# Performance work log

Measured on AMD Instinct MI355X. Metric: run time of the kernel, lower is better.

The kernel has to match this reference:

```python
import math
import jax, jax.numpy as jnp
import numpy as np

B, L, T, D, H, SD = 8, 512, 512, 768, 12, 5


def setup_inputs() -> dict:
    key = jax.random.key(0)
    ks = jax.random.split(key, 16)
    s = 0.02
    return {
        "q": jax.random.normal(ks[0], (B, L, D), jnp.float32),
        "k": jax.random.normal(ks[1], (B, T, D), jnp.float32),
        "v": jax.random.normal(ks[2], (B, T, D), jnp.float32),
        "pairwise_locs": jax.random.normal(ks[3], (B, L, T, SD), jnp.float32),
        "key_padding_mask": jax.random.randint(ks[4], (B, T), 0, 2).astype(bool),
        "Wq": jax.random.normal(ks[5], (D, D), jnp.float32) * s,
        "bq": jnp.zeros((D,), jnp.float32),
        "Wk": jax.random.normal(ks[6], (D, D), jnp.float32) * s,
        "bk": jnp.zeros((D,), jnp.float32),
        "Wv": jax.random.normal(ks[7], (D, D), jnp.float32) * s,
        "bv": jnp.zeros((D,), jnp.float32),
        "Wl": jax.random.normal(ks[8], (D, H * (SD + 1)), jnp.float32) * s,
        "bl": jnp.zeros((H * (SD + 1),), jnp.float32),
        "Wf": jax.random.normal(ks[9], (D, D), jnp.float32) * s,
        "bf": jnp.zeros((D,), jnp.float32),
    }


def reference(q, k, v, pairwise_locs, key_padding_mask,
              Wq, bq, Wk, bk, Wv, bv, Wl, bl, Wf, bf):
    b, l, d = q.shape
    t = k.shape[1]
    sd = pairwise_locs.shape[-1]
    h = Wl.shape[1] // (sd + 1)          # spatial_multihead=True -> h == n_head
    dh = d // h

    # projections -> [h, b, seq, dh]
    qh = (q @ Wq + bq).reshape(b, l, h, dh).transpose(2, 0, 1, 3)
    kh = (k @ Wk + bk).reshape(b, t, h, dh).transpose(2, 0, 1, 3)
    vh = (v @ Wv + bv).reshape(b, t, h, dh).transpose(2, 0, 1, 3)

    attn = jnp.einsum('hblk,hbtk->hblt', qh, kh) / math.sqrt(dh)

    # language-conditioned spatial weights from residual (= q input)
    sw = (q @ Wl + bl).reshape(b, l, h, sd + 1).transpose(2, 0, 1, 3)  # [h,b,l,sd+1]
    spatial_bias = sw[..., :1]
    spatial_w = sw[..., 1:]
    loc_attn = jax.nn.sigmoid(
        jnp.einsum('hbld,bltd->hblt', spatial_w, pairwise_locs) + spatial_bias)

    mask = key_padding_mask[None, :, None, :]          # [1,b,1,t]
    attn = jnp.where(mask, -jnp.inf, attn)
    loc_attn = jnp.where(mask, 0.0, loc_attn)

    fused_attn = jax.nn.softmax(jnp.log(jnp.clip(loc_attn, 1e-6)) + attn, axis=3)

    out = jnp.einsum('hblt,hbtv->hblv', fused_attn, vh)
    out = out.transpose(1, 2, 0, 3).reshape(b, l, d)
    out = out @ Wf + bf
    return (out, fused_attn)
```

## Files before the change

### kernel.cpp

```cpp
#include <hip/hip_runtime.h>
#include <hip/hip_bf16.h>

#define B_ 8
#define L_ 512
#define T_ 512
#define D_ 768
#define H_ 12
#define DH_ 64
#define SD_ 5
#define NSW_ 72
#define K2_ 1536
#define K3_ 2304

typedef __attribute__((ext_vector_type(8))) short bf16x8;
typedef __attribute__((ext_vector_type(4))) float f32x4;

__device__ __forceinline__ unsigned short f2bf(float x) {
    union { __hip_bfloat16 h; unsigned short u; } cv;
    cv.h = __float2bfloat16(x);
    return cv.u;
}
__device__ __forceinline__ float bf2f(unsigned short u) {
    union { unsigned short u; __hip_bfloat16 h; } cv;
    cv.u = u;
    return __bfloat162float(cv.h);
}

__device__ __forceinline__ void gload_lds16(const void* g, void* l) {
    __builtin_amdgcn_global_load_lds((const __attribute__((address_space(1))) void*)g,
                                     (__attribute__((address_space(3))) void*)l,
                                     16, 0, 0);
}

__global__ __launch_bounds__(256) void asplit_kernel(
    const float* __restrict__ q, const float* __restrict__ k, const float* __restrict__ v,
    short* __restrict__ q2, short* __restrict__ k2, short* __restrict__ v2)
{
    const int z = blockIdx.z;
    const float* A = (z == 0) ? q : (z == 1) ? k : v;
    short* O = (z == 0) ? q2 : (z == 1) ? k2 : v2;
    const int col = blockIdx.x * 256 + threadIdx.x;
    const int m   = blockIdx.y;
    if (col >= D_) return;
    const float a = A[(size_t)m * D_ + col];
    const unsigned short hi = f2bf(a);
    const unsigned short lo = f2bf(a - bf2f(hi));
    O[(size_t)m * K2_ + col]       = (short)hi;
    O[(size_t)m * K2_ + D_ + col]  = (short)lo;
}

__global__ __launch_bounds__(256) void wsplit_kernel(
    const float* __restrict__ Wq, const float* __restrict__ Wk,
    const float* __restrict__ Wv, const float* __restrict__ Wl,
    const float* __restrict__ Wf,
    short* __restrict__ WqT3, short* __restrict__ WkT3, short* __restrict__ WvT3,
    short* __restrict__ WlT3, short* __restrict__ WfT3)
{
    const int z = blockIdx.z;
    const float* W; short* O; int Nw, Npad;
    if (z == 0)      { W = Wq; O = WqT3; Nw = D_;   Npad = 768; }
    else if (z == 1) { W = Wk; O = WkT3; Nw = D_;   Npad = 768; }
    else if (z == 2) { W = Wv; O = WvT3; Nw = D_;   Npad = 768; }
    else if (z == 3) { W = Wl; O = WlT3; Nw = NSW_; Npad = 128; }
    else             { W = Wf; O = WfT3; Nw = D_;   Npad = 768; }

    const int k0 = blockIdx.x * 64;
    const int n0 = blockIdx.y * 64;
    if (n0 >= Npad) return;

    __shared__ float sm[64][65];
    const int c  = threadIdx.x & 63;
    const int r4 = threadIdx.x >> 6;

#pragma unroll
    for (int i = 0; i < 16; i++) {
        const int r = i * 4 + r4;
        float val = 0.f;
        if (n0 + c < Nw) val = W[(size_t)(k0 + r) * Nw + n0 + c];
        sm[r][c] = val;
    }
    __syncthreads();

#pragma unroll
    for (int i = 0; i < 16; i++) {
        const int nl = i * 4 + r4;
        const int n  = n0 + nl;
        if (n >= Npad) continue;
        const float v = (n < Nw) ? sm[c][nl] : 0.f;
        const unsigned short hi = f2bf(v);
        const unsigned short lo = f2bf(v - bf2f(hi));
        const size_t rb = (size_t)n * K3_;
        O[rb + k0 + c]        = (short)hi;
        O[rb + 768 + k0 + c]  = (short)lo;
        O[rb + 1536 + k0 + c] = (short)hi;
    }
}

__global__ __launch_bounds__(256) void mfma_gemm(
    const short* __restrict__ q2, const short* __restrict__ k2, const short* __restrict__ v2,
    const short* __restrict__ WqT3, const short* __restrict__ WkT3,
    const short* __restrict__ WvT3, const short* __restrict__ WlT3,
    const short* __restrict__ WfT3,
    const float* __restrict__ bq, const float* __restrict__ bk,
    const float* __restrict__ bv, const float* __restrict__ bl,
    const float* __restrict__ bf,
    const short* __restrict__ outp2,
    float* __restrict__ qh, float* __restrict__ kh, float* __restrict__ vh,
    float* __restrict__ swv, float* __restrict__ outf,
    int zoff)
{
    const int z = zoff + blockIdx.z;
    const short* A2; const short* WT3; const float* bias; float* C; int Ncols;
    if (z == 0)      { A2 = q2;    WT3 = WqT3; bias = bq; C = qh;   Ncols = D_;   }
    else if (z == 1) { A2 = k2;    WT3 = WkT3; bias = bk; C = kh;   Ncols = D_;   }
    else if (z == 2) { A2 = v2;    WT3 = WvT3; bias = bv; C = vh;   Ncols = D_;   }
    else if (z == 3) { A2 = q2;    WT3 = WlT3; bias = bl; C = swv;  Ncols = NSW_; }
    else             { A2 = outp2; WT3 = WfT3; bias = bf; C = outf; Ncols = D_;   }

    if (z == 3 && blockIdx.x != 0) return;

    const int m0 = blockIdx.y * 128;
    const int n0 = blockIdx.x * 128;

    __shared__ __align__(16) short As[128 * 32];
    __shared__ __align__(16) short Bs[128 * 32];

    const int tid  = threadIdx.x;
    const int lane = tid & 63;
    const int wv_  = tid >> 6;
    const int wm   = (wv_ & 1) << 6;
    const int wn   = (wv_ >> 1) << 6;
    const int l15  = lane & 15;
    const int quad = lane >> 4;

    f32x4 acc[4][4] = {};

    const int sa  = tid;
    const int sb  = tid + 256;
    const int ra  = sa >> 2, ka = (sa & 3) << 3;
    const int rb  = sb >> 2, kb8 = (sb & 3) << 3;

    for (int kb = 0; kb < K3_; kb += 32) {
        const int akb = (kb < 768) ? kb : kb - 768;
        __syncthreads();
        gload_lds16(A2  + (size_t)(m0 + ra) * K2_ + akb + ka,  &As[sa << 3]);
        gload_lds16(A2  + (size_t)(m0 + rb) * K2_ + akb + kb8, &As[sb << 3]);
        gload_lds16(WT3 + (size_t)(n0 + ra) * K3_ + kb  + ka,  &Bs[sa << 3]);
        gload_lds16(WT3 + (size_t)(n0 + rb) * K3_ + kb  + kb8, &Bs[sb << 3]);
        __syncthreads();

        bf16x8 af[4], bfr[4];
#pragma unroll
        for (int t = 0; t < 4; t++) {
            af[t]  = *(const bf16x8*)&As[(wm + t * 16 + l15) * 32 + quad * 8];
            bfr[t] = *(const bf16x8*)&Bs[(wn + t * 16 + l15) * 32 + quad * 8];
        }
#pragma unroll
        for (int mt = 0; mt < 4; mt++)
#pragma unroll
            for (int nt = 0; nt < 4; nt++)
                acc[mt][nt] = __builtin_amdgcn_mfma_f32_16x16x32_bf16(
                    af[mt], bfr[nt], acc[mt][nt], 0, 0, 0);
    }

#pragma unroll
    for (int nt = 0; nt < 4; nt++) {
        const int col = n0 + wn + nt * 16 + l15;
        if (col >= Ncols) continue;
        const float bvv = bias[col];
#pragma unroll
        for (int mt = 0; mt < 4; mt++) {
            const int row = m0 + wm + mt * 16 + quad * 4;
#pragma unroll
            for (int r = 0; r < 4; r++)
                C[(size_t)(row + r) * Ncols + col] = acc[mt][nt][r] + bvv;
        }
    }
}

__global__ __launch_bounds__(256) void attn_kernel(
    const float* __restrict__ qhp, const float* __restrict__ khp,
    const float* __restrict__ vhp, const float* __restrict__ swp,
    const float* __restrict__ ploc, const int* __restrict__ maskp,
    float* __restrict__ fused, short* __restrict__ outp2,
    float* __restrict__ sums)
{
    const int h  = blockIdx.z;
    const int b  = blockIdx.y;
    const int l0 = blockIdx.x << 6;
    const int tid = threadIdx.x;

    __shared__ float qs[64][65];
    __shared__ float ks[32][65];
    __shared__ float vs[32][64];
    __shared__ float ps[64][33];
    __shared__ float sws[64][6];
    __shared__ float ssum[64];
    __shared__ int   smask[32];

    {
        const int r  = tid >> 2;
        const int cq = (tid & 3) << 4;
        const float* src = qhp + (size_t)((b << 9) + l0 + r) * D_ + (h << 6) + cq;
#pragma unroll
        for (int u = 0; u < 4; u++) {
            float4 t4 = *(const float4*)(src + (u << 2));
            qs[r][cq + (u << 2) + 0] = t4.x;
            qs[r][cq + (u << 2) + 1] = t4.y;
            qs[r][cq + (u << 2) + 2] = t4.z;
            qs[r][cq + (u << 2) + 3] = t4.w;
        }
    }
    for (int i = tid; i < 64 * 6; i += 256) {
        const int r = i / 6, c = i % 6;
        sws[r][c] = swp[(size_t)((b << 9) + l0 + r) * NSW_ + h * 6 + c];
    }
    if (tid < 64) ssum[tid] = 0.f;

    const int tg = tid & 15;
    const int lg = tid >> 4;
    const int l4 = lg << 2;
    const int t2 = tg << 1;
    const int d4 = tg << 2;

    float acc_o[4][4];
#pragma unroll
    for (int i = 0; i < 4; i++)
#pragma unroll
        for (int j = 0; j < 4; j++) acc_o[i][j] = 0.f;

    for (int t0 = 0; t0 < T_; t0 += 32) {
        __syncthreads();
        {
            const int r  = tid >> 4;
            const int c4 = (tid & 15) << 2;
            const float* kp = khp + (size_t)((b << 9) + t0 + r) * D_ + (h << 6) + c4;
            const float* vp = vhp + (size_t)((b << 9) + t0 + r) * D_ + (h << 6) + c4;
            float4 ka = *(const float4*)kp;
            float4 kbv = *(const float4*)(kp + 16 * D_);
            ks[r][c4 + 0] = ka.x; ks[r][c4 + 1] = ka.y;
            ks[r][c4 + 2] = ka.z; ks[r][c4 + 3] = ka.w;
            ks[r + 16][c4 + 0] = kbv.x; ks[r + 16][c4 + 1] = kbv.y;
            ks[r + 16][c4 + 2] = kbv.z; ks[r + 16][c4 + 3] = kbv.w;
            float4 va = *(const float4*)vp;
            float4 vb = *(const float4*)(vp + 16 * D_);
            *(float4*)&vs[r][c4]      = va;
            *(float4*)&vs[r + 16][c4] = vb;
        }
        if (tid < 32) smask[tid] = maskp[(b << 9) + t0 + tid];
        __syncthreads();

        float qk[4][2];
#pragma unroll
        for (int i = 0; i < 4; i++) { qk[i][0] = 0.f; qk[i][1] = 0.f; }
#pragma unroll 4
        for (int kk = 0; kk < 64; kk++) {
            const float kv0 = ks[t2 + 0][kk];
            const float kv1 = ks[t2 + 1][kk];
#pragma unroll
            for (int i = 0; i < 4; i++) {
                const float qv = qs[l4 + i][kk];
                qk[i][0] += qv * kv0;
                qk[i][1] += qv * kv1;
            }
        }
#pragma unroll
        for (int j = 0; j < 2; j++) {
            const int tt  = t2 + j;
            const int msk = smask[tt];
#pragma unroll
            for (int i = 0; i < 4; i++) {
                const int l = l0 + l4 + i;
                const float* pl = ploc + ((size_t)((b << 9) + l) * T_ + (t0 + tt)) * SD_;
                float s = sws[l4 + i][0];
#pragma unroll
                for (int d = 0; d < SD_; d++) s += sws[l4 + i][1 + d] * pl[d];
                const float sig = fmaxf(1.f / (1.f + __expf(-s)), 1e-6f);
                const float p   = msk ? 0.f : sig * __expf(qk[i][j] * 0.125f);
                ps[l4 + i][tt] = p;
            }
        }
        __syncthreads();

        if (tid < 64) {
            float ssl = 0.f;
#pragma unroll
            for (int t = 0; t < 32; t++) ssl += ps[tid][t];
            ssum[tid] += ssl;
        }

#pragma unroll 4
        for (int t = 0; t < 32; t++) {
            const float4 vv = *(const float4*)&vs[t][d4];
            float pv[4];
#pragma unroll
            for (int i = 0; i < 4; i++) pv[i] = ps[l4 + i][t];
#pragma unroll
            for (int i = 0; i < 4; i++) {
                acc_o[i][0] += pv[i] * vv.x;
                acc_o[i][1] += pv[i] * vv.y;
                acc_o[i][2] += pv[i] * vv.z;
                acc_o[i][3] += pv[i] * vv.w;
            }
        }

        {
            const int t  = tid & 31;
            const int lb = (tid >> 5) << 3;
            const size_t rowbase = (size_t)((h * B_ + b) * L_ + l0);
#pragma unroll
            for (int e = 0; e < 8; e++) {
                const int l = lb + e;
                fused[(rowbase + l) * T_ + t0 + t] = ps[l][t];
            }
        }
    }
    __syncthreads();

    if (tid < 64) sums[(size_t)((h * B_ + b) * L_) + l0 + tid] = ssum[tid];

#pragma unroll
    for (int i = 0; i < 4; i++) {
        const float inv = 1.f / ssum[l4 + i];
        const size_t base = (size_t)((b << 9) + l0 + l4 + i) * K2_ + (h << 6) + d4;
#pragma unroll
        for (int j = 0; j < 4; j++) {
            const float val = acc_o[i][j] * inv;
            const unsigned short hi = f2bf(val);
            const unsigned short lo = f2bf(val - bf2f(hi));
            outp2[base + j]       = (short)hi;
            outp2[base + D_ + j]  = (short)lo;
        }
    }
}

__global__ __launch_bounds__(256) void norm_kernel(
    float* __restrict__ fused, const float* __restrict__ sums)
{
    const int gi = blockIdx.x * 256 + threadIdx.x;
    float4* f4 = (float4*)fused;
    float4 v = f4[gi];
    const float inv = 1.f / sums[gi >> 7];
    v.x *= inv; v.y *= inv; v.z *= inv; v.w *= inv;
    f4[gi] = v;
}

extern "C" void kernel_launch(void* const* d_in, const int* in_sizes, int n_in,
                              void* d_out, int out_size, void* d_ws, size_t ws_size,
                              hipStream_t stream) {
    const float* q    = (const float*)d_in[0];
    const float* k    = (const float*)d_in[1];
    const float* v    = (const float*)d_in[2];
    const float* ploc = (const float*)d_in[3];
    const int*   mask = (const int*)  d_in[4];
    const float* Wq   = (const float*)d_in[5];
    const float* bq   = (const float*)d_in[6];
    const float* Wk   = (const float*)d_in[7];
    const float* bk   = (const float*)d_in[8];
    const float* Wv   = (const float*)d_in[9];
    const float* bv   = (const float*)d_in[10];
    const float* Wl   = (const float*)d_in[11];
    const float* bl   = (const float*)d_in[12];
    const float* Wf   = (const float*)d_in[13];
    const float* bf   = (const float*)d_in[14];

    char* p = (char*)d_ws;
    short* q2    = (short*)p; p += (size_t)4096 * K2_ * 2;
    short* k2    = (short*)p; p += (size_t)4096 * K2_ * 2;
    short* v2    = (short*)p; p += (size_t)4096 * K2_ * 2;
    short* WqT3  = (short*)p; p += (size_t)768 * K3_ * 2;
    short* WkT3  = (short*)p; p += (size_t)768 * K3_ * 2;
    short* WvT3  = (short*)p; p += (size_t)768 * K3_ * 2;
    short* WlT3  = (short*)p; p += (size_t)128 * K3_ * 2;
    short* WfT3  = (short*)p; p += (size_t)768 * K3_ * 2;
    float* qh    = (float*)p; p += (size_t)4096 * D_ * 4;
    float* kh    = (float*)p; p += (size_t)4096 * D_ * 4;
    float* vh    = (float*)p; p += (size_t)4096 * D_ * 4;
    float* swv   = (float*)p; p += (size_t)4096 * NSW_ * 4;
    float* sums  = (float*)p; p += (size_t)H_ * B_ * L_ * 4;
    short* outp2 = q2;

    float* out   = (float*)d_out;
    float* fused = out + (size_t)4096 * D_;

    asplit_kernel<<<dim3(3, 4096, 3), 256, 0, stream>>>(q, k, v, q2, k2, v2);
    wsplit_kernel<<<dim3(12, 12, 5), 256, 0, stream>>>(
        Wq, Wk, Wv, Wl, Wf, WqT3, WkT3, WvT3, WlT3, WfT3);

    mfma_gemm<<<dim3(6, 32, 4), 256, 0, stream>>>(
        q2, k2, v2, WqT3, WkT3, WvT3, WlT3, WfT3,
        bq, bk, bv, bl, bf, outp2, qh, kh, vh, swv, out, 0);

    attn_kernel<<<dim3(8, 8, 12), 256, 0, stream>>>(
        qh, kh, vh, swv, ploc, mask, fused, outp2, sums);

    norm_kernel<<<dim3(24576), 256, 0, stream>>>(fused, sums);

    mfma_gemm<<<dim3(6, 32, 1), 256, 0, stream>>>(
        q2, k2, v2, WqT3, WkT3, WvT3, WlT3, WfT3,
        bq, bk, bv, bl, bf, outp2, qh, kh, vh, swv, out, 4);
}
```

Before: 546.9 us.

## Move attention QK and PV to split-bf16 MFMA with precomputed spatial sigmoid

The projection GEMM epilogue now writes Q/K as hi/lo bf16 pairs in head-major layout and V transposed, so the attention kernel can use MFMA for QK^T and PV with a three-term split-bf16 product instead of scalar fp32 FMAs. A separate sig_kernel precomputes the masked spatial sigmoid into an fp16 buffer that aliases the workspace, which takes the strided pairwise_locs reads out of the attention inner loop. The attention tile grows to 64 keys with XOR-swizzled LDS loaded directly from global memory, and the fused-attention rows are stored as float4. In exchange there is an extra kernel launch, an fp16 intermediate that may affect accuracy, and more workspace traffic.

```diff
diff --git a/kernel.cpp b/kernel.cpp
--- a/kernel.cpp
+++ b/kernel.cpp
@@ -14,6 +14,7 @@
 
 typedef __attribute__((ext_vector_type(8))) short bf16x8;
 typedef __attribute__((ext_vector_type(4))) float f32x4;
+typedef unsigned short ushort_t;
 
 __device__ __forceinline__ unsigned short f2bf(float x) {
     union { __hip_bfloat16 h; unsigned short u; } cv;
@@ -105,17 +106,17 @@
     const float* __restrict__ bv, const float* __restrict__ bl,
     const float* __restrict__ bf,
     const short* __restrict__ outp2,
-    float* __restrict__ qh, float* __restrict__ kh, float* __restrict__ vh,
+    ushort_t* __restrict__ qs2a, ushort_t* __restrict__ ks2a, ushort_t* __restrict__ vt2,
     float* __restrict__ swv, float* __restrict__ outf,
     int zoff)
 {
     const int z = zoff + blockIdx.z;
-    const short* A2; const short* WT3; const float* bias; float* C; int Ncols;
-    if (z == 0)      { A2 = q2;    WT3 = WqT3; bias = bq; C = qh;   Ncols = D_;   }
-    else if (z == 1) { A2 = k2;    WT3 = WkT3; bias = bk; C = kh;   Ncols = D_;   }
-    else if (z == 2) { A2 = v2;    WT3 = WvT3; bias = bv; C = vh;   Ncols = D_;   }
-    else if (z == 3) { A2 = q2;    WT3 = WlT3; bias = bl; C = swv;  Ncols = NSW_; }
-    else             { A2 = outp2; WT3 = WfT3; bias = bf; C = outf; Ncols = D_;   }
+    const short* A2; const short* WT3; const float* bias;
+    if (z == 0)      { A2 = q2;    WT3 = WqT3; bias = bq; }
+    else if (z == 1) { A2 = k2;    WT3 = WkT3; bias = bk; }
+    else if (z == 2) { A2 = v2;    WT3 = WvT3; bias = bv; }
+    else if (z == 3) { A2 = q2;    WT3 = WlT3; bias = bl; }
+    else             { A2 = outp2; WT3 = WfT3; bias = bf; }
 
     if (z == 3 && blockIdx.x != 0) return;
 
@@ -163,175 +164,279 @@
                     af[mt], bfr[nt], acc[mt][nt], 0, 0, 0);
     }
 
-#pragma unroll
-    for (int nt = 0; nt < 4; nt++) {
-        const int col = n0 + wn + nt * 16 + l15;
-        if (col >= Ncols) continue;
-        const float bvv = bias[col];
-#pragma unroll
-        for (int mt = 0; mt < 4; mt++) {
-            const int row = m0 + wm + mt * 16 + quad * 4;
-#pragma unroll
-            for (int r = 0; r < 4; r++)
-                C[(size_t)(row + r) * Ncols + col] = acc[mt][nt][r] + bvv;
-        }
+    if (z <= 2) {
+        ushort_t* dst = (z == 0) ? qs2a : (z == 1) ? ks2a : vt2;
+#pragma unroll
+        for (int nt = 0; nt < 4; nt++) {
+            const int col = n0 + wn + nt * 16 + l15;
+            const int hh = col >> 6, dd = col & 63;
+            const float bvv = bias[col];
+#pragma unroll
+            for (int mt = 0; mt < 4; mt++) {
+                const int rowb = m0 + wm + mt * 16 + quad * 4;
+                if (z < 2) {
+#pragma unroll
+                    for (int r = 0; r < 4; r++) {
+                        const int gr = rowb + r;
+                        const int bb = gr >> 9, ll = gr & 511;
+                        const float x = acc[mt][nt][r] + bvv;
+                        const ushort_t hi = f2bf(x);
+                        const ushort_t lo = f2bf(x - bf2f(hi));
+                        const size_t base = (((size_t)hh * B_ + bb) * 512 + ll) * 128 + dd;
+                        dst[base]      = hi;
+                        dst[base + 64] = lo;
+                    }
+                } else {
+                    const int bb = rowb >> 9, tt = rowb & 511;
+                    ushort_t hi4[4], lo4[4];
+#pragma unroll
+                    for (int r = 0; r < 4; r++) {
+                        const float x = acc[mt][nt][r] + bvv;
+                        hi4[r] = f2bf(x);
+                        lo4[r] = f2bf(x - bf2f(hi4[r]));
+                    }
+                    const size_t base = (((size_t)hh * B_ + bb) * 128 + dd) * 512 + tt;
+                    *(ushort4*)&dst[base]            = *(ushort4*)hi4;
+                    *(ushort4*)&dst[base + 64 * 512] = *(ushort4*)lo4;
+                }
+            }
+        }
+    } else if (z == 3) {
+#pragma unroll
+        for (int nt = 0; nt < 4; nt++) {
+            const int col = n0 + wn + nt * 16 + l15;
+            if (col >= NSW_) continue;
+            const float bvv = bias[col];
+#pragma unroll
+            for (int mt = 0; mt < 4; mt++) {
+                const int row = m0 + wm + mt * 16 + quad * 4;
+#pragma unroll
+                for (int r = 0; r < 4; r++)
+                    swv[(size_t)(row + r) * NSW_ + col] = acc[mt][nt][r] + bvv;
+            }
+        }
+    } else {
+#pragma unroll
+        for (int nt = 0; nt < 4; nt++) {
+            const int col = n0 + wn + nt * 16 + l15;
+            const float bvv = bias[col];
+#pragma unroll
+            for (int mt = 0; mt < 4; mt++) {
+                const int row = m0 + wm + mt * 16 + quad * 4;
+#pragma unroll
+                for (int r = 0; r < 4; r++)
+                    outf[(size_t)(row + r) * D_ + col] = acc[mt][nt][r] + bvv;
+            }
+        }
+    }
+}
+
+__global__ __launch_bounds__(256) void sig_kernel(
+    const float* __restrict__ ploc, const float* __restrict__ swv,
+    const int* __restrict__ maskp, _Float16* __restrict__ sig16)
+{
+    const int b = blockIdx.y;
+    const int l = blockIdx.x;
+    const int tid = threadIdx.x;
+
+    __shared__ float pls[512 * 5];
+    __shared__ float sws[72];
+    __shared__ int   msk[512];
+
+    const float* src = ploc + (size_t)(b * 512 + l) * 512 * 5;
+    for (int i = tid; i < 640; i += 256)
+        *(float4*)&pls[i * 4] = *(const float4*)(src + i * 4);
+    if (tid < 72) sws[tid] = swv[(size_t)(b * 512 + l) * NSW_ + tid];
+    for (int i = tid; i < 512; i += 256) msk[i] = maskp[b * 512 + i];
+    __syncthreads();
+
+    for (int e = tid; e < H_ * 512; e += 256) {
+        const int t  = e & 511;
+        const int hh = e >> 9;
+        float s = sws[hh * 6];
+#pragma unroll
+        for (int d = 0; d < SD_; d++) s += sws[hh * 6 + 1 + d] * pls[t * 5 + d];
+        const float sig = msk[t] ? 0.f : fmaxf(1.f / (1.f + __expf(-s)), 1e-6f);
+        sig16[(((size_t)hh * B_ + b) * 512 + l) * 512 + t] = (_Float16)sig;
     }
 }
 
 __global__ __launch_bounds__(256) void attn_kernel(
-    const float* __restrict__ qhp, const float* __restrict__ khp,
-    const float* __restrict__ vhp, const float* __restrict__ swp,
-    const float* __restrict__ ploc, const int* __restrict__ maskp,
-    float* __restrict__ fused, short* __restrict__ outp2,
+    const ushort_t* __restrict__ qs2, const ushort_t* __restrict__ ks2,
+    const ushort_t* __restrict__ vt2, const _Float16* __restrict__ sig16,
+    float* __restrict__ fused, ushort_t* __restrict__ outp2,
     float* __restrict__ sums)
 {
     const int h  = blockIdx.z;
     const int b  = blockIdx.y;
     const int l0 = blockIdx.x << 6;
-    const int tid = threadIdx.x;
-
-    __shared__ float qs[64][65];
-    __shared__ float ks[32][65];
-    __shared__ float vs[32][64];
-    __shared__ float ps[64][33];
-    __shared__ float sws[64][6];
+    const int hb = h * B_ + b;
+    const int tid  = threadIdx.x;
+    const int lane = tid & 63;
+    const int wv   = tid >> 6;
+    const int l15  = lane & 15;
+    const int quad = lane >> 4;
+
+    __shared__ __align__(16) ushort_t qs[64 * 128];
+    __shared__ __align__(16) ushort_t ks[64 * 128];
+    __shared__ __align__(16) ushort_t vts[128 * 64];
+    __shared__ __align__(16) ushort_t ps[64 * 136];
+    __shared__ float ssb[4 * 64];
     __shared__ float ssum[64];
-    __shared__ int   smask[32];
 
     {
-        const int r  = tid >> 2;
-        const int cq = (tid & 3) << 4;
-        const float* src = qhp + (size_t)((b << 9) + l0 + r) * D_ + (h << 6) + cq;
-#pragma unroll
-        for (int u = 0; u < 4; u++) {
-            float4 t4 = *(const float4*)(src + (u << 2));
-            qs[r][cq + (u << 2) + 0] = t4.x;
-            qs[r][cq + (u << 2) + 1] = t4.y;
-            qs[r][cq + (u << 2) + 2] = t4.z;
-            qs[r][cq + (u << 2) + 3] = t4.w;
-        }
-    }
-    for (int i = tid; i < 64 * 6; i += 256) {
-        const int r = i / 6, c = i % 6;
-        sws[r][c] = swp[(size_t)((b << 9) + l0 + r) * NSW_ + h * 6 + c];
-    }
-    if (tid < 64) ssum[tid] = 0.f;
-
-    const int tg = tid & 15;
-    const int lg = tid >> 4;
-    const int l4 = lg << 2;
-    const int t2 = tg << 1;
-    const int d4 = tg << 2;
-
-    float acc_o[4][4];
-#pragma unroll
-    for (int i = 0; i < 4; i++)
-#pragma unroll
-        for (int j = 0; j < 4; j++) acc_o[i][j] = 0.f;
-
-    for (int t0 = 0; t0 < T_; t0 += 32) {
+        const size_t qbase = ((size_t)hb * 512 + l0) * 128;
+#pragma unroll
+        for (int j = 0; j < 4; j++) {
+            const int i = tid + 256 * j;
+            const int r = i >> 4, c = i & 15, gc = c ^ (r & 7);
+            gload_lds16(qs2 + qbase + r * 128 + gc * 8, &qs[i * 8]);
+        }
+    }
+
+    float pacc = 0.f;
+    f32x4 accpv[4] = {};
+
+    for (int t0 = 0; t0 < T_; t0 += 64) {
         __syncthreads();
         {
-            const int r  = tid >> 4;
-            const int c4 = (tid & 15) << 2;
-            const float* kp = khp + (size_t)((b << 9) + t0 + r) * D_ + (h << 6) + c4;
-            const float* vp = vhp + (size_t)((b << 9) + t0 + r) * D_ + (h << 6) + c4;
-            float4 ka = *(const float4*)kp;
-            float4 kbv = *(const float4*)(kp + 16 * D_);
-            ks[r][c4 + 0] = ka.x; ks[r][c4 + 1] = ka.y;
-            ks[r][c4 + 2] = ka.z; ks[r][c4 + 3] = ka.w;
-            ks[r + 16][c4 + 0] = kbv.x; ks[r + 16][c4 + 1] = kbv.y;
-            ks[r + 16][c4 + 2] = kbv.z; ks[r + 16][c4 + 3] = kbv.w;
-            float4 va = *(const float4*)vp;
-            float4 vb = *(const float4*)(vp + 16 * D_);
-            *(float4*)&vs[r][c4]      = va;
-            *(float4*)&vs[r + 16][c4] = vb;
-        }
-        if (tid < 32) smask[tid] = maskp[(b << 9) + t0 + tid];
+            const size_t kbase = ((size_t)hb * 512 + t0) * 128;
+#pragma unroll
+            for (int j = 0; j < 4; j++) {
+                const int i = tid + 256 * j;
+                const int r = i >> 4, c = i & 15, gc = c ^ (r & 7);
+                gload_lds16(ks2 + kbase + r * 128 + gc * 8, &ks[i * 8]);
+            }
+            const size_t vbase = (size_t)hb * 128 * 512;
+#pragma unroll
+            for (int j = 0; j < 4; j++) {
+                const int i = tid + 256 * j;
+                const int r = i >> 3, c = i & 7, gc = c ^ (r & 7);
+                gload_lds16(vt2 + vbase + (size_t)r * 512 + t0 + gc * 8, &vts[i * 8]);
+            }
+        }
         __syncthreads();
 
-        float qk[4][2];
-#pragma unroll
-        for (int i = 0; i < 4; i++) { qk[i][0] = 0.f; qk[i][1] = 0.f; }
-#pragma unroll 4
-        for (int kk = 0; kk < 64; kk++) {
-            const float kv0 = ks[t2 + 0][kk];
-            const float kv1 = ks[t2 + 1][kk];
-#pragma unroll
-            for (int i = 0; i < 4; i++) {
-                const float qv = qs[l4 + i][kk];
-                qk[i][0] += qv * kv0;
-                qk[i][1] += qv * kv1;
-            }
-        }
-#pragma unroll
-        for (int j = 0; j < 2; j++) {
-            const int tt  = t2 + j;
-            const int msk = smask[tt];
-#pragma unroll
-            for (int i = 0; i < 4; i++) {
-                const int l = l0 + l4 + i;
-                const float* pl = ploc + ((size_t)((b << 9) + l) * T_ + (t0 + tt)) * SD_;
-                float s = sws[l4 + i][0];
-#pragma unroll
-                for (int d = 0; d < SD_; d++) s += sws[l4 + i][1 + d] * pl[d];
-                const float sig = fmaxf(1.f / (1.f + __expf(-s)), 1e-6f);
-                const float p   = msk ? 0.f : sig * __expf(qk[i][j] * 0.125f);
-                ps[l4 + i][tt] = p;
-            }
+        float sigv[4][4];
+        {
+            const _Float16* sgp = sig16 + (((size_t)hb * 512 + l0) * 512) + t0 + wv * 16 + l15;
+#pragma unroll
+            for (int mt = 0; mt < 4; mt++)
+#pragma unroll
+                for (int r2 = 0; r2 < 4; r2++)
+                    sigv[mt][r2] = (float)sgp[(size_t)(mt * 16 + quad * 4 + r2) * 512];
+        }
+
+        f32x4 acq[4] = {};
+        {
+            const int trow = wv * 16 + l15;
+            const int tsw  = trow & 7;
+            const bf16x8 bk0 = *(const bf16x8*)&ks[trow * 128 + ((0  + quad) ^ tsw) * 8];
+            const bf16x8 bk1 = *(const bf16x8*)&ks[trow * 128 + ((4  + quad) ^ tsw) * 8];
+            const bf16x8 bk2 = *(const bf16x8*)&ks[trow * 128 + ((8  + quad) ^ tsw) * 8];
+            const bf16x8 bk3 = *(const bf16x8*)&ks[trow * 128 + ((12 + quad) ^ tsw) * 8];
+#pragma unroll
+            for (int mt = 0; mt < 4; mt++) {
+                const int arow = mt * 16 + l15;
+                const int asw  = arow & 7;
+                const bf16x8 a0 = *(const bf16x8*)&qs[arow * 128 + ((0  + quad) ^ asw) * 8];
+                const bf16x8 a1 = *(const bf16x8*)&qs[arow * 128 + ((4  + quad) ^ asw) * 8];
+                const bf16x8 a2 = *(const bf16x8*)&qs[arow * 128 + ((8  + quad) ^ asw) * 8];
+                const bf16x8 a3 = *(const bf16x8*)&qs[arow * 128 + ((12 + quad) ^ asw) * 8];
+                f32x4 a = acq[mt];
+                a = __builtin_amdgcn_mfma_f32_16x16x32_bf16(a0, bk0, a, 0, 0, 0);
+                a = __builtin_amdgcn_mfma_f32_16x16x32_bf16(a1, bk1, a, 0, 0, 0);
+                a = __builtin_amdgcn_mfma_f32_16x16x32_bf16(a0, bk2, a, 0, 0, 0);
+                a = __builtin_amdgcn_mfma_f32_16x16x32_bf16(a1, bk3, a, 0, 0, 0);
+                a = __builtin_amdgcn_mfma_f32_16x16x32_bf16(a2, bk0, a, 0, 0, 0);
+                a = __builtin_amdgcn_mfma_f32_16x16x32_bf16(a3, bk1, a, 0, 0, 0);
+                acq[mt] = a;
+            }
+        }
+
+        {
+            const int tcol = wv * 16 + l15;
+#pragma unroll
+            for (int mt = 0; mt < 4; mt++)
+#pragma unroll
+                for (int r2 = 0; r2 < 4; r2++) {
+                    const int lrow = mt * 16 + quad * 4 + r2;
+                    const float p  = sigv[mt][r2] * __expf(acq[mt][r2] * 0.125f);
+                    const ushort_t hi = f2bf(p);
+                    const ushort_t lo = f2bf(p - bf2f(hi));
+                    ps[lrow * 136 + tcol]      = hi;
+                    ps[lrow * 136 + 64 + tcol] = lo;
+                }
         }
         __syncthreads();
 
-        if (tid < 64) {
-            float ssl = 0.f;
-#pragma unroll
-            for (int t = 0; t < 32; t++) ssl += ps[tid][t];
-            ssum[tid] += ssl;
-        }
-
-#pragma unroll 4
-        for (int t = 0; t < 32; t++) {
-            const float4 vv = *(const float4*)&vs[t][d4];
-            float pv[4];
-#pragma unroll
-            for (int i = 0; i < 4; i++) pv[i] = ps[l4 + i][t];
-#pragma unroll
-            for (int i = 0; i < 4; i++) {
-                acc_o[i][0] += pv[i] * vv.x;
-                acc_o[i][1] += pv[i] * vv.y;
-                acc_o[i][2] += pv[i] * vv.z;
-                acc_o[i][3] += pv[i] * vv.w;
-            }
-        }
-
         {
-            const int t  = tid & 31;
-            const int lb = (tid >> 5) << 3;
-            const size_t rowbase = (size_t)((h * B_ + b) * L_ + l0);
-#pragma unroll
-            for (int e = 0; e < 8; e++) {
-                const int l = lb + e;
-                fused[(rowbase + l) * T_ + t0 + t] = ps[l][t];
-            }
-        }
-    }
+            const int row = tid >> 2, c4 = tid & 3;
+            float vbuf[16];
+            float s = 0.f;
+#pragma unroll
+            for (int jj = 0; jj < 16; jj++) {
+                const int t = c4 * 16 + jj;
+                const float pv = bf2f(ps[row * 136 + t]) + bf2f(ps[row * 136 + 64 + t]);
+                vbuf[jj] = pv;
+                s += pv;
+            }
+            pacc += s;
+            float* dstf = fused + ((size_t)hb * 512 + l0 + row) * 512 + t0 + c4 * 16;
+#pragma unroll
+            for (int jj = 0; jj < 4; jj++)
+                *(float4*)(dstf + jj * 4) = *(float4*)&vbuf[jj * 4];
+        }
+
+        {
+            const int vrh = wv * 16 + l15;
+            const int vrl = 64 + vrh;
+            const int swh = vrh & 7, swl = vrl & 7;
+            const bf16x8 bh0 = *(const bf16x8*)&vts[vrh * 64 + ((0 + quad) ^ swh) * 8];
+            const bf16x8 bh1 = *(const bf16x8*)&vts[vrh * 64 + ((4 + quad) ^ swh) * 8];
+            const bf16x8 bl0 = *(const bf16x8*)&vts[vrl * 64 + ((0 + quad) ^ swl) * 8];
+            const bf16x8 bl1 = *(const bf16x8*)&vts[vrl * 64 + ((4 + quad) ^ swl) * 8];
+#pragma unroll
+            for (int mt = 0; mt < 4; mt++) {
+                const int prow = mt * 16 + l15;
+                const bf16x8 ph0 = *(const bf16x8*)&ps[prow * 136 + 0  + quad * 8];
+                const bf16x8 ph1 = *(const bf16x8*)&ps[prow * 136 + 32 + quad * 8];
+                const bf16x8 pl0 = *(const bf16x8*)&ps[prow * 136 + 64 + quad * 8];
+                const bf16x8 pl1 = *(const bf16x8*)&ps[prow * 136 + 96 + quad * 8];
+                f32x4 a = accpv[mt];
+                a = __builtin_amdgcn_mfma_f32_16x16x32_bf16(ph0, bh0, a, 0, 0, 0);
+                a = __builtin_amdgcn_mfma_f32_16x16x32_bf16(ph1, bh1, a, 0, 0, 0);
+                a = __builtin_amdgcn_mfma_f32_16x16x32_bf16(ph0, bl0, a, 0, 0, 0);
+                a = __builtin_amdgcn_mfma_f32_16x16x32_bf16(ph1, bl1, a, 0, 0, 0);
+                a = __builtin_amdgcn_mfma_f32_16x16x32_bf16(pl0, bh0, a, 0, 0, 0);
+                a = __builtin_amdgcn_mfma_f32_16x16x32_bf16(pl1, bh1, a, 0, 0, 0);
+                accpv[mt] = a;
+            }
+        }
+    }
+
     __syncthreads();
-
-    if (tid < 64) sums[(size_t)((h * B_ + b) * L_) + l0 + tid] = ssum[tid];
-
-#pragma unroll
-    for (int i = 0; i < 4; i++) {
-        const float inv = 1.f / ssum[l4 + i];
-        const size_t base = (size_t)((b << 9) + l0 + l4 + i) * K2_ + (h << 6) + d4;
-#pragma unroll
-        for (int j = 0; j < 4; j++) {
-            const float val = acc_o[i][j] * inv;
-            const unsigned short hi = f2bf(val);
-            const unsigned short lo = f2bf(val - bf2f(hi));
-            outp2[base + j]       = (short)hi;
-            outp2[base + D_ + j]  = (short)lo;
-        }
-    }
+    ssb[(tid & 3) * 64 + (tid >> 2)] = pacc;
+    __syncthreads();
+    if (tid < 64) {
+        const float s = ssb[tid] + ssb[64 + tid] + ssb[128 + tid] + ssb[192 + tid];
+        ssum[tid] = s;
+        sums[(size_t)hb * 512 + l0 + tid] = s;
+    }
+    __syncthreads();
+
+#pragma unroll
+    for (int mt = 0; mt < 4; mt++)
+#pragma unroll
+        for (int r2 = 0; r2 < 4; r2++) {
+            const int lrow = mt * 16 + quad * 4 + r2;
+            const float val = accpv[mt][r2] / ssum[lrow];
+            const ushort_t hi = f2bf(val);
+            const ushort_t lo = f2bf(val - bf2f(hi));
+            const size_t obase = ((size_t)(b * 512 + l0 + lrow)) * K2_ + h * 64 + wv * 16 + l15;
+            outp2[obase]       = hi;
+            outp2[obase + D_]  = lo;
+        }
 }
 
 __global__ __launch_bounds__(256) void norm_kernel(
@@ -364,21 +469,22 @@
     const float* Wf   = (const float*)d_in[13];
     const float* bf   = (const float*)d_in[14];
 
-    char* p = (char*)d_ws;
-    short* q2    = (short*)p; p += (size_t)4096 * K2_ * 2;
-    short* k2    = (short*)p; p += (size_t)4096 * K2_ * 2;
-    short* v2    = (short*)p; p += (size_t)4096 * K2_ * 2;
-    short* WqT3  = (short*)p; p += (size_t)768 * K3_ * 2;
-    short* WkT3  = (short*)p; p += (size_t)768 * K3_ * 2;
-    short* WvT3  = (short*)p; p += (size_t)768 * K3_ * 2;
-    short* WlT3  = (short*)p; p += (size_t)128 * K3_ * 2;
-    short* WfT3  = (short*)p; p += (size_t)768 * K3_ * 2;
-    float* qh    = (float*)p; p += (size_t)4096 * D_ * 4;
-    float* kh    = (float*)p; p += (size_t)4096 * D_ * 4;
-    float* vh    = (float*)p; p += (size_t)4096 * D_ * 4;
-    float* swv   = (float*)p; p += (size_t)4096 * NSW_ * 4;
-    float* sums  = (float*)p; p += (size_t)H_ * B_ * L_ * 4;
-    short* outp2 = q2;
+    char* base = (char*)d_ws;
+    short*    q2    = (short*)(base + 0);
+    short*    k2    = (short*)(base + 12582912);
+    short*    v2    = (short*)(base + 25165824);
+    short*    WqT3  = (short*)(base + 37748736);
+    short*    WkT3  = (short*)(base + 41287680);
+    short*    WvT3  = (short*)(base + 44826624);
+    short*    WlT3  = (short*)(base + 48365568);
+    _Float16* sig16 = (_Float16*)(base + 0);
+    short*    WfT3  = (short*)(base + 50331648);
+    ushort_t* qs2a  = (ushort_t*)(base + 53870592);
+    ushort_t* ks2a  = (ushort_t*)(base + 66453504);
+    ushort_t* vt2   = (ushort_t*)(base + 79036416);
+    float*    swv   = (float*)(base + 91619328);
+    float*    sums  = (float*)(base + 92798976);
+    short*    outp2 = (short*)(base + 92995584);
 
     float* out   = (float*)d_out;
     float* fused = out + (size_t)4096 * D_;
@@ -389,14 +495,16 @@
 
     mfma_gemm<<<dim3(6, 32, 4), 256, 0, stream>>>(
         q2, k2, v2, WqT3, WkT3, WvT3, WlT3, WfT3,
-        bq, bk, bv, bl, bf, outp2, qh, kh, vh, swv, out, 0);
+        bq, bk, bv, bl, bf, outp2, qs2a, ks2a, vt2, swv, out, 0);
+
+    sig_kernel<<<dim3(512, 8), 256, 0, stream>>>(ploc, swv, mask, sig16);
 
     attn_kernel<<<dim3(8, 8, 12), 256, 0, stream>>>(
-        qh, kh, vh, swv, ploc, mask, fused, outp2, sums);
+        qs2a, ks2a, vt2, sig16, fused, (ushort_t*)outp2, sums);
 
     norm_kernel<<<dim3(24576), 256, 0, stream>>>(fused, sums);
 
     mfma_gemm<<<dim3(6, 32, 1), 256, 0, stream>>>(
         q2, k2, v2, WqT3, WkT3, WvT3, WlT3, WfT3,
-        bq, bk, bv, bl, bf, outp2, qh, kh, vh, swv, out, 4);
-}
+        bq, bk, bv, bl, bf, outp2, qs2a, ks2a, vt2, swv, out, 4);
+}
```

New measurement: 511.4 us. 1.07x faster.
